# Kernel tuning notes

Hardware: AMD Instinct MI355X
Metric: run time of the kernel (lower is better)

## Reference

```python
import jax, jax.numpy as jnp
import numpy as np

NEG_INF = -1e9
B, D, T_MEL, T_TEXT = 16, 192, 2048, 512


def setup_inputs() -> dict:
    key = jax.random.key(0)
    k1, k2, k3, k4, k5 = jax.random.split(key, 5)
    z_p = jax.random.normal(k1, (B, D, T_MEL), dtype=jnp.float32)
    m_p = jax.random.normal(k2, (B, D, T_TEXT), dtype=jnp.float32)
    logs_p = 0.1 * jax.random.normal(k3, (B, D, T_TEXT), dtype=jnp.float32)
    phoneme_lengths = jax.random.randint(k4, (B,), T_TEXT // 2, T_TEXT + 1, dtype=jnp.int32)
    mel_lengths = jax.random.randint(k5, (B,), T_MEL // 2, T_MEL + 1, dtype=jnp.int32)
    return {"z_p": z_p, "m_p": m_p, "logs_p": logs_p,
            "phoneme_lengths": phoneme_lengths, "mel_lengths": mel_lengths}


def neg_cent_matrix(z_p, m_p, logs_p):
    # z_p: [B,D,Ty] (mel frames), m_p/logs_p: [B,D,Tx] (phonemes)
    s = jnp.exp(-2.0 * logs_p)                                             # 1/sigma^2, [B,D,Tx]
    nc1 = jnp.sum(-0.5 * jnp.log(2.0 * jnp.pi) - logs_p, axis=1, keepdims=True)  # [B,1,Tx]
    nc2 = jnp.einsum('bdy,bdx->byx', -0.5 * z_p * z_p, s)                  # [B,Ty,Tx]
    nc3 = jnp.einsum('bdy,bdx->byx', z_p, m_p * s)                         # [B,Ty,Tx]
    nc4 = jnp.sum(-0.5 * m_p * m_p * s, axis=1, keepdims=True)             # [B,1,Tx]
    return nc1 + nc2 + nc3 + nc4                                           # [B,Ty,Tx]


def maximum_path(neg_cent, t_xs, t_ys):
    """Monotonic alignment search (VITS maximum_path), vmapped over batch.

    neg_cent: [B, T_y, T_x] log-likelihood scores; t_xs/t_ys: valid lengths.
    Returns hard alignment path [B, T_y, T_x] in {0,1}.
    """
    _, T_y, T_x = neg_cent.shape
    x_idx = jnp.arange(T_x)

    def single(value, t_x, t_y):
        # forward DP: cum[y,x] = value[y,x] + max(cum[y-1,x], cum[y-1,x-1])
        init = jnp.where(x_idx == 0, value[0], NEG_INF)

        def fwd_step(prev, v_row):
            shifted = jnp.concatenate([jnp.full((1,), NEG_INF, prev.dtype), prev[:-1]])
            cur = v_row + jnp.maximum(prev, shifted)
            return cur, cur

        _, rest = jax.lax.scan(fwd_step, init, value[1:])
        cum = jnp.concatenate([init[None, :], rest], axis=0)               # [T_y,T_x]

        # backtrack from (t_y-1, t_x-1); rows with y >= t_y are inactive (zeros)
        def bwd_step(index, y):
            active = y < t_y
            row = ((x_idx == index) & active).astype(value.dtype)
            prev_row = cum[jnp.maximum(y - 1, 0)]
            move = (index == y) | (prev_row[index] < prev_row[jnp.maximum(index - 1, 0)])
            move = move & (index > 0) & active & (y > 0)
            nxt = jnp.where(active, index - move.astype(index.dtype), index)
            return nxt, row

        _, rows = jax.lax.scan(bwd_step, t_x - 1, jnp.arange(T_y)[::-1])
        return rows[::-1]

    return jax.vmap(single)(neg_cent, t_xs, t_ys)


def reference(z_p, m_p, logs_p, phoneme_lengths, mel_lengths):
    neg_cent = neg_cent_matrix(z_p, m_p, logs_p)                           # [B,Ty,Tx]
    attn = maximum_path(neg_cent, phoneme_lengths, mel_lengths)            # [B,Ty,Tx]
    T_x = m_p.shape[-1]
    ph_mask = (jnp.arange(T_x)[None, :] < phoneme_lengths[:, None]).astype(z_p.dtype)[:, None, :]  # [B,1,Tx]
    w = jnp.sum(attn, axis=1)[:, None, :]                                  # durations, [B,1,Tx]
    logw_ = jnp.log(w + 1e-6) * ph_mask                                    # [B,1,Tx]
    return neg_cent, attn, logw_
```

## Files before the change

kernel.cpp:

```cpp
#include <hip/hip_runtime.h>
#include <cstdint>
#include <cstddef>

#define B_   16
#define D_   192
#define TY   2048
#define TX   512
#define NEG_INF_F (-1e9f)

#define CHUNK 16
#define RING  4
#define WAVES 8

#define WAITVM(N)  __builtin_amdgcn_s_waitcnt(((N) & 15) | (7 << 4) | (15 << 8) | (((N) >> 4) << 14))
#define WAITLGKM0  __builtin_amdgcn_s_waitcnt(15 | (7 << 4) | (0 << 8) | (3 << 14))

__device__ __forceinline__ void gload_lds16(const float* g, float* l) {
    __builtin_amdgcn_global_load_lds(
        (const __attribute__((address_space(1))) void*)g,
        (__attribute__((address_space(3))) void*)l, 16, 0, 0);
}

__device__ __forceinline__ float dpp_shr1_neginf(float x) {
    int xi  = __builtin_bit_cast(int, x);
    int old = __builtin_bit_cast(int, NEG_INF_F);
    int r = __builtin_amdgcn_update_dpp(old, xi, 0x138, 0xF, 0xF, false);
    return __builtin_bit_cast(float, r);
}

__global__ __launch_bounds__(256)
void nc14_kernel(const float* __restrict__ m_p,
                 const float* __restrict__ logs_p,
                 float* __restrict__ nc14) {
    int gid = blockIdx.x * 256 + threadIdx.x;
    int b = gid >> 9;
    int x = gid & 511;
    const float c = -0.9189385332046727f;
    const float* lp = logs_p + (size_t)b * D_ * TX + x;
    const float* mp = m_p    + (size_t)b * D_ * TX + x;
    float acc1 = 0.f, acc2 = 0.f;
    for (int d = 0; d < D_; ++d) {
        float l = lp[(size_t)d * TX];
        float m = mp[(size_t)d * TX];
        float s = __expf(-2.f * l);
        acc1 += c - l;
        acc2 += m * m * s;
    }
    nc14[gid] = acc1 - 0.5f * acc2;
}

#define BM 128
#define BN 128
#define BK 16

__global__ __launch_bounds__(512)
void gemm_kernel(const float* __restrict__ z_p,
                 const float* __restrict__ m_p,
                 const float* __restrict__ logs_p,
                 const float* __restrict__ nc14,
                 float* __restrict__ out) {
    __shared__ float a_z [BK][BM];
    __shared__ float a_z2[BK][BM];
    __shared__ float sb_s [BK][BN];
    __shared__ float sb_ms[BK][BN];

    const int b  = blockIdx.z;
    const int m0 = blockIdx.y * BM;
    const int n0 = blockIdx.x * BN;
    const int tid = threadIdx.x;
    const int tx = tid & 31;
    const int ty = tid >> 5;

    const int skk = tid >> 5;
    const int sy  = (tid & 31) * 4;

    const float* zb = z_p    + (size_t)b * D_ * TY;
    const float* mb = m_p    + (size_t)b * D_ * TX;
    const float* lb = logs_p + (size_t)b * D_ * TX;

    float acc[8][4];
    #pragma unroll
    for (int i = 0; i < 8; ++i)
        #pragma unroll
        for (int j = 0; j < 4; ++j) acc[i][j] = 0.f;

    float4 va, vlg, vmm;
    auto ld = [&](int k0) {
        va  = *(const float4*)(zb + (size_t)(k0 + skk) * TY + m0 + sy);
        vlg = *(const float4*)(lb + (size_t)(k0 + skk) * TX + n0 + sy);
        vmm = *(const float4*)(mb + (size_t)(k0 + skk) * TX + n0 + sy);
    };
    auto st = [&]() {
        *(float4*)&a_z[skk][sy] = va;
        float4 w;
        w.x = -0.5f * va.x * va.x; w.y = -0.5f * va.y * va.y;
        w.z = -0.5f * va.z * va.z; w.w = -0.5f * va.w * va.w;
        *(float4*)&a_z2[skk][sy] = w;
        float4 s;
        s.x = __expf(-2.f * vlg.x); s.y = __expf(-2.f * vlg.y);
        s.z = __expf(-2.f * vlg.z); s.w = __expf(-2.f * vlg.w);
        *(float4*)&sb_s[skk][sy] = s;
        float4 ms;
        ms.x = vmm.x * s.x; ms.y = vmm.y * s.y;
        ms.z = vmm.z * s.z; ms.w = vmm.w * s.w;
        *(float4*)&sb_ms[skk][sy] = ms;
    };

    ld(0);
    for (int k0 = 0; k0 < D_; k0 += BK) {
        st();
        __syncthreads();
        if (k0 + BK < D_) ld(k0 + BK);
        #pragma unroll
        for (int kk = 0; kk < BK; ++kk) {
            float az[8], a2[8], bs[4], bm[4];
            *(float4*)&az[0] = *(const float4*)&a_z [kk][ty * 8];
            *(float4*)&az[4] = *(const float4*)&a_z [kk][ty * 8 + 4];
            *(float4*)&a2[0] = *(const float4*)&a_z2[kk][ty * 8];
            *(float4*)&a2[4] = *(const float4*)&a_z2[kk][ty * 8 + 4];
            *(float4*)&bs[0] = *(const float4*)&sb_s [kk][tx * 4];
            *(float4*)&bm[0] = *(const float4*)&sb_ms[kk][tx * 4];
            #pragma unroll
            for (int i = 0; i < 8; ++i)
                #pragma unroll
                for (int j = 0; j < 4; ++j)
                    acc[i][j] += a2[i] * bs[j] + az[i] * bm[j];
        }
        __syncthreads();
    }
    const float4 c4 = *(const float4*)(nc14 + b * TX + n0 + tx * 4);
    float* ob = out + (size_t)b * TY * TX + (size_t)m0 * TX + n0 + tx * 4;
    #pragma unroll
    for (int i = 0; i < 8; ++i) {
        float4 r;
        r.x = acc[i][0] + c4.x; r.y = acc[i][1] + c4.y;
        r.z = acc[i][2] + c4.z; r.w = acc[i][3] + c4.w;
        *(float4*)(ob + (size_t)(ty * 8 + i) * TX) = r;
    }
}

__global__ __launch_bounds__(512, 1)
void dp_kernel(float* __restrict__ out,
               const int* __restrict__ t_xs,
               const int* __restrict__ t_ys,
               int* __restrict__ cumE) {
    const size_t PLANE = (size_t)TY * TX;
    const size_t OFF1  = (size_t)B_ * PLANE;
    const size_t OFF2  = 2 * OFF1;

    __shared__ float rows_lds[WAVES][RING][CHUNK * 64];
    __shared__ float bnd[RING][WAVES + 1][CHUNK];
    __shared__ int   w_lds[TX];

    const int b    = blockIdx.x;
    const int tid  = threadIdx.x;
    const int w    = tid >> 6;
    const int lane = tid & 63;
    const int t_x  = t_xs[b];
    const int t_y  = t_ys[b];
    const int tym1 = t_y - 1;
    const int NC   = (t_y + CHUNK - 1) / CHUNK;

    const float* nc   = out + (size_t)b * PLANE;
    float*       attn = out + OFF1 + (size_t)b * PLANE;
    float*       logw = out + OFF2 + (size_t)b * TX;
    unsigned char* bitsb = (unsigned char*)attn;

    w_lds[tid] = 0;
    {
        float* bf = &bnd[0][0][0];
        if (tid < 512) bf[tid] = NEG_INF_F;
        if (tid < 64)  bf[512 + tid] = NEG_INF_F;
    }

    auto issue_chunk = [&](int c) {
        const int slot = c % RING;
        #pragma unroll
        for (int k = 0; k < CHUNK / 4; ++k) {
            int y = c * CHUNK + 4 * k + (lane >> 4);
            if (y > tym1) y = tym1;
            const float* gp = nc + (size_t)y * TX + 64 * w + 4 * (lane & 15);
            gload_lds16(gp, &rows_lds[w][slot][k * 256]);
        }
    };

    float cl = NEG_INF_F;
    const bool lane0  = (lane == 0);
    const bool lane63 = (lane == 63);

    issue_chunk(0);
    issue_chunk(1);
    issue_chunk(2);

    const int ITERS = NC + WAVES - 1;
    for (int i = 0; i < ITERS; ++i) {
        WAITLGKM0;
        __asm__ volatile("" ::: "memory");
        __builtin_amdgcn_s_barrier();
        __asm__ volatile("" ::: "memory");
        const int c = i - w;
        if (c < 0 || c >= NC) continue;
        const bool full = (c + 3 < NC);
        if (full) issue_chunk(c + 3);

        const int pc = c % RING;
        float4 bq0 = *(const float4*)&bnd[pc][w][0];
        float4 bq1 = *(const float4*)&bnd[pc][w][4];
        float4 bq2 = *(const float4*)&bnd[pc][w][8];
        float4 bq3 = *(const float4*)&bnd[pc][w][12];
        float carry = bnd[(c + RING - 1) % RING][w][CHUNK - 1];
        float bv[CHUNK] = {carry,
                           bq0.x, bq0.y, bq0.z, bq0.w,
                           bq1.x, bq1.y, bq1.z, bq1.w,
                           bq2.x, bq2.y, bq2.z, bq2.w,
                           bq3.x, bq3.y, bq3.z};

        if (c >= 3) {
            if (full)               { WAITVM(15); }
            else if (c + 3 == NC)   { WAITVM(11); }
            else if (c + 2 == NC)   { WAITVM(7);  }
            else                    { WAITVM(3);  }
        } else {
            if (c == 0)             { WAITVM(12); }
            else if (c == 1)        { WAITVM(13); }
            else                    { WAITVM(14); }
        }
        __asm__ volatile("" ::: "memory");

        #pragma unroll
        for (int r = 0; r < CHUNK; ++r) __asm__ volatile("" : "+v"(bv[r]));

        const float* vrow = &rows_lds[w][pc][0];
        float vv[CHUNK];
        #pragma unroll
        for (int r = 0; r < CHUNK; ++r) vv[r] = vrow[r * 64 + lane];
        #pragma unroll
        for (int r = 0; r < CHUNK; ++r) __asm__ volatile("" : "+v"(vv[r]));

        const int ybase = c * CHUNK;
        float pub[CHUNK];
        unsigned mlo = 0, mhi = 0;
        #pragma unroll
        for (int r = 0; r < CHUNK; ++r) {
            float sh = dpp_shr1_neginf(cl);
            sh = lane0 ? bv[r] : sh;
            unsigned long long mk = __ballot(cl < sh);
            float cn = vv[r] + fmaxf(cl, sh);
            if (r == 0) {
                float iv = (w == 0 && lane0) ? vv[0] : NEG_INF_F;
                cn = (ybase == 0) ? iv : cn;
            }
            cl = cn;
            pub[r] = cl;
            unsigned lo32 = (unsigned)mk;
            unsigned hi32 = (unsigned)(mk >> 32);
            bool sel = (lane == r);
            mlo = sel ? lo32 : mlo;
            mhi = sel ? hi32 : mhi;
        }
        if (lane63) {
            *(float4*)&bnd[pc][w + 1][0]  = make_float4(pub[0],  pub[1],  pub[2],  pub[3]);
            *(float4*)&bnd[pc][w + 1][4]  = make_float4(pub[4],  pub[5],  pub[6],  pub[7]);
            *(float4*)&bnd[pc][w + 1][8]  = make_float4(pub[8],  pub[9],  pub[10], pub[11]);
            *(float4*)&bnd[pc][w + 1][12] = make_float4(pub[12], pub[13], pub[14], pub[15]);
        }
        {
            const int ys = ybase + lane;
            if (lane < CHUNK && ys < t_y)
                *(uint2*)(bitsb + (size_t)ys * 64 + 8 * w) = make_uint2(mlo, mhi);
        }
    }

    __builtin_amdgcn_s_waitcnt(0);
    __asm__ volatile("" ::: "memory");
    __builtin_amdgcn_s_barrier();
    __asm__ volatile("" ::: "memory");
    if (w != 0) return;

    int idx  = t_x - 1;
    int yhi  = tym1;
    int ytop = tym1;
    int wh   = idx >> 5;

    unsigned vlo = 0, vhi = 0;
    {
        int cnt0 = (ytop >= 31) ? 32 : (ytop + 1);
        int wlo = (wh > 0) ? wh - 1 : 0;
        if (lane < cnt0) {
            const unsigned* rp = (const unsigned*)(bitsb + (size_t)(ytop - lane) * 64);
            vlo = rp[wlo];
            vhi = rp[wh];
        }
    }
    while (ytop >= 0) {
        const int cnt = (ytop >= 31) ? 32 : (ytop + 1);
        unsigned p0 = 0, p1 = 0, p2 = 0;
        const int ynext = ytop - cnt;
        if (ynext >= 0 && lane < 32) {
            int rr = ynext - lane; if (rr < 0) rr = 0;
            const unsigned* rp = (const unsigned*)(bitsb + (size_t)rr * 64);
            const int w2i = wh;
            const int w1i = (wh > 0) ? wh - 1 : 0;
            const int w0i = (wh > 1) ? wh - 2 : 0;
            p0 = rp[w0i]; p1 = rp[w1i]; p2 = rp[w2i];
        }
        const int base  = ((wh > 0) ? wh - 1 : 0) * 32;
        const int idx0  = idx;
        const int yhi0  = yhi;
        unsigned  mask  = 0;
        auto step = [&](int i2) {
            int yy = ytop - i2;
            unsigned lo = (unsigned)__builtin_amdgcn_readlane((int)vlo, i2);
            unsigned hi = (unsigned)__builtin_amdgcn_readlane((int)vhi, i2);
            unsigned long long V = ((unsigned long long)hi << 32) | lo;
            int pos   = idx - base;
            int bit   = (int)((V >> pos) & 1ull);
            int force = (idx == yy) ? 1 : 0;
            int move  = (force | bit) & ((idx > 0) ? 1 : 0) & ((yy > 0) ? 1 : 0);
            mask |= ((unsigned)move) << i2;
            yhi  = move ? (yy - 1) : yhi;
            idx -= move;
        };
        if (cnt == 32) {
            #pragma unroll
            for (int i2 = 0; i2 < 32; ++i2) step(i2);
        } else {
            for (int i2 = 0; i2 < cnt; ++i2) step(i2);
        }
        {
            const int k = lane;
            if (k < 32 && ((mask >> k) & 1u)) {
                unsigned pri = mask & ((1u << k) - 1u);
                int m  = __popc(pri);
                int ph = idx0 - m;
                int dur;
                if (pri) { int kp = 31 - __builtin_clz(pri); dur = k - kp; }
                else     { dur = yhi0 - ytop + k + 1; }
                w_lds[ph] = dur;
            }
        }
        ytop -= cnt;
        if (ytop >= 0) {
            const int whn = idx >> 5;
            vlo = (whn == wh) ? p1 : p0;
            vhi = (whn == wh) ? p2 : p1;
            wh = whn;
        }
    }
    if (lane0) w_lds[idx] = yhi + 1;

    __asm__ volatile("" ::: "memory");
    int v2[8];
    int run = 0;
    #pragma unroll
    for (int j = 0; j < 8; ++j) {
        int wv = w_lds[lane * 8 + j];
        run += wv;
        v2[j] = run;
    }
    int off = run;
    #pragma unroll
    for (int d = 1; d < 64; d <<= 1) {
        int t = __shfl_up(off, d, 64);
        if (lane >= d) off += t;
    }
    int excl = off - run;
    #pragma unroll
    for (int j = 0; j < 8; ++j) {
        int x = lane * 8 + j;
        cumE[b * TX + x] = v2[j] + excl;
        int wv = w_lds[x];
        logw[x] = (x < t_x) ? logf((float)wv + 1e-6f) : 0.f;
    }
}

__global__ __launch_bounds__(256)
void attn_fill_kernel(const int* __restrict__ cumE,
                      float* __restrict__ out) {
    const size_t PLANE = (size_t)TY * TX;
    const size_t OFF1  = (size_t)B_ * PLANE;
    __shared__ int cs[TX + 1];
    const int b  = blockIdx.y;
    const int y0 = blockIdx.x * 4;
    const int t  = threadIdx.x;
    if (t == 0) cs[0] = 0;
    cs[1 + t]       = cumE[b * TX + t];
    cs[1 + 256 + t] = cumE[b * TX + 256 + t];
    __syncthreads();
    const int y  = y0 + (t >> 6);
    const int x0 = (t & 63) * 8;
    float r[8];
    #pragma unroll
    for (int j = 0; j < 8; ++j)
        r[j] = (cs[x0 + j] <= y && y < cs[x0 + j + 1]) ? 1.f : 0.f;
    float* p = out + OFF1 + (size_t)b * PLANE + (size_t)y * TX + x0;
    *(float4*)p       = *(float4*)&r[0];
    *(float4*)(p + 4) = *(float4*)&r[4];
}

extern "C" void kernel_launch(void* const* d_in, const int* in_sizes, int n_in,
                              void* d_out, int out_size, void* d_ws, size_t ws_size,
                              hipStream_t stream) {
    const float* z_p    = (const float*)d_in[0];
    const float* m_p    = (const float*)d_in[1];
    const float* logs_p = (const float*)d_in[2];
    const int* ph_len   = (const int*)d_in[3];
    const int* mel_len  = (const int*)d_in[4];
    float* out  = (float*)d_out;
    float* nc14 = (float*)d_ws;
    int*   cumE = (int*)d_ws;

    nc14_kernel<<<(B_ * TX) / 256, 256, 0, stream>>>(m_p, logs_p, nc14);
    gemm_kernel<<<dim3(TX / BN, TY / BM, B_), 512, 0, stream>>>(z_p, m_p, logs_p, nc14, out);
    dp_kernel<<<B_, WAVES * 64, 0, stream>>>(out, ph_len, mel_len, cumE);
    attn_fill_kernel<<<dim3(TY / 4, B_), 256, 0, stream>>>(cumE, out);
}
```

Baseline: 701.8 us.

## Prefetch next chunk's LDS rows and carry into registers during current DP step

The forward DP loop now double-buffers the per-chunk value rows and the carry value in two register arrays. After computing the current chunk, each wave waits for the next chunk's global-to-LDS load and reads it into the alternate register set, so LDS read latency is moved off the critical path at the start of the next iteration. The loop is unrolled by two with swapped buffers, and the vmcnt wait thresholds are retuned to match the new issue order. This costs extra VGPRs and adds risk in the correctness of the wait counts and of reading the carry before the barrier.

```diff
diff --git a/kernel.cpp b/kernel.cpp
--- a/kernel.cpp
+++ b/kernel.cpp
@@ -192,82 +192,108 @@
     issue_chunk(1);
     issue_chunk(2);
 
+    float vvA[CHUNK], vvB[CHUNK];
+    float carryA = NEG_INF_F, carryB = NEG_INF_F;
+    #pragma unroll
+    for (int r = 0; r < CHUNK; ++r) { vvA[r] = 0.f; vvB[r] = 0.f; }
+
+    if (w == 0) {
+        WAITVM(8);
+        __asm__ volatile("" ::: "memory");
+        const float* vn = &rows_lds[0][0][0];
+        #pragma unroll
+        for (int r = 0; r < CHUNK; ++r) vvA[r] = vn[r * 64 + lane];
+        #pragma unroll
+        for (int r = 0; r < CHUNK; ++r) __asm__ volatile("" : "+v"(vvA[r]));
+    }
+
     const int ITERS = NC + WAVES - 1;
-    for (int i = 0; i < ITERS; ++i) {
+
+    auto body = [&](float (&vvc)[CHUNK], float& carryc,
+                    float (&vvn)[CHUNK], float& carryn, int i) {
         WAITLGKM0;
         __asm__ volatile("" ::: "memory");
         __builtin_amdgcn_s_barrier();
         __asm__ volatile("" ::: "memory");
         const int c = i - w;
-        if (c < 0 || c >= NC) continue;
-        const bool full = (c + 3 < NC);
-        if (full) issue_chunk(c + 3);
-
-        const int pc = c % RING;
-        float4 bq0 = *(const float4*)&bnd[pc][w][0];
-        float4 bq1 = *(const float4*)&bnd[pc][w][4];
-        float4 bq2 = *(const float4*)&bnd[pc][w][8];
-        float4 bq3 = *(const float4*)&bnd[pc][w][12];
-        float carry = bnd[(c + RING - 1) % RING][w][CHUNK - 1];
-        float bv[CHUNK] = {carry,
-                           bq0.x, bq0.y, bq0.z, bq0.w,
-                           bq1.x, bq1.y, bq1.z, bq1.w,
-                           bq2.x, bq2.y, bq2.z, bq2.w,
-                           bq3.x, bq3.y, bq3.z};
-
-        if (c >= 3) {
-            if (full)               { WAITVM(15); }
-            else if (c + 3 == NC)   { WAITVM(11); }
-            else if (c + 2 == NC)   { WAITVM(7);  }
+        if (c >= 0 && c < NC) {
+            if (c + 3 < NC) issue_chunk(c + 3);
+            const int pc = c % RING;
+            float4 bq0 = *(const float4*)&bnd[pc][w][0];
+            float4 bq1 = *(const float4*)&bnd[pc][w][4];
+            float4 bq2 = *(const float4*)&bnd[pc][w][8];
+            float4 bq3 = *(const float4*)&bnd[pc][w][12];
+
+            const int ybase = c * CHUNK;
+            float pub[CHUNK];
+            unsigned mlo = 0, mhi = 0;
+            {
+                float sh = dpp_shr1_neginf(cl);
+                sh = lane0 ? carryc : sh;
+                unsigned long long mk = __ballot(cl < sh);
+                float cn = vvc[0] + fmaxf(cl, sh);
+                if (ybase == 0)
+                    cn = (w == 0 && lane0) ? vvc[0] : NEG_INF_F;
+                cl = cn;
+                pub[0] = cl;
+                bool sel = (lane == 0);
+                mlo = sel ? (unsigned)mk : mlo;
+                mhi = sel ? (unsigned)(mk >> 32) : mhi;
+            }
+            float bv1[CHUNK - 1] = {bq0.x, bq0.y, bq0.z, bq0.w,
+                                    bq1.x, bq1.y, bq1.z, bq1.w,
+                                    bq2.x, bq2.y, bq2.z, bq2.w,
+                                    bq3.x, bq3.y, bq3.z};
+            #pragma unroll
+            for (int r = 1; r < CHUNK; ++r) {
+                float sh = dpp_shr1_neginf(cl);
+                sh = lane0 ? bv1[r - 1] : sh;
+                unsigned long long mk = __ballot(cl < sh);
+                float cn = vvc[r] + fmaxf(cl, sh);
+                cl = cn;
+                pub[r] = cl;
+                bool sel = (lane == r);
+                mlo = sel ? (unsigned)mk : mlo;
+                mhi = sel ? (unsigned)(mk >> 32) : mhi;
+            }
+            if (lane63) {
+                *(float4*)&bnd[pc][w + 1][0]  = make_float4(pub[0],  pub[1],  pub[2],  pub[3]);
+                *(float4*)&bnd[pc][w + 1][4]  = make_float4(pub[4],  pub[5],  pub[6],  pub[7]);
+                *(float4*)&bnd[pc][w + 1][8]  = make_float4(pub[8],  pub[9],  pub[10], pub[11]);
+                *(float4*)&bnd[pc][w + 1][12] = make_float4(pub[12], pub[13], pub[14], pub[15]);
+            }
+            {
+                const int ys = ybase + lane;
+                if (lane < CHUNK && ys < t_y)
+                    *(uint2*)(bitsb + (size_t)ys * 64 + 8 * w) = make_uint2(mlo, mhi);
+            }
+        }
+        const int cp = (i - w) + 1;
+        if (cp >= 0 && cp < NC) {
+            const int cc = cp - 1;
+            if (cp == 0)            { WAITVM(8);  }
+            else if (cp == 1)       { WAITVM(9);  }
+            else if (cp == 2)       { WAITVM(10); }
+            else if (cc + 4 <= NC)  { WAITVM(11); }
+            else if (cc + 3 == NC)  { WAITVM(7);  }
             else                    { WAITVM(3);  }
-        } else {
-            if (c == 0)             { WAITVM(12); }
-            else if (c == 1)        { WAITVM(13); }
-            else                    { WAITVM(14); }
-        }
-        __asm__ volatile("" ::: "memory");
-
-        #pragma unroll
-        for (int r = 0; r < CHUNK; ++r) __asm__ volatile("" : "+v"(bv[r]));
-
-        const float* vrow = &rows_lds[w][pc][0];
-        float vv[CHUNK];
-        #pragma unroll
-        for (int r = 0; r < CHUNK; ++r) vv[r] = vrow[r * 64 + lane];
-        #pragma unroll
-        for (int r = 0; r < CHUNK; ++r) __asm__ volatile("" : "+v"(vv[r]));
-
-        const int ybase = c * CHUNK;
-        float pub[CHUNK];
-        unsigned mlo = 0, mhi = 0;
-        #pragma unroll
-        for (int r = 0; r < CHUNK; ++r) {
-            float sh = dpp_shr1_neginf(cl);
-            sh = lane0 ? bv[r] : sh;
-            unsigned long long mk = __ballot(cl < sh);
-            float cn = vv[r] + fmaxf(cl, sh);
-            if (r == 0) {
-                float iv = (w == 0 && lane0) ? vv[0] : NEG_INF_F;
-                cn = (ybase == 0) ? iv : cn;
-            }
-            cl = cn;
-            pub[r] = cl;
-            unsigned lo32 = (unsigned)mk;
-            unsigned hi32 = (unsigned)(mk >> 32);
-            bool sel = (lane == r);
-            mlo = sel ? lo32 : mlo;
-            mhi = sel ? hi32 : mhi;
-        }
-        if (lane63) {
-            *(float4*)&bnd[pc][w + 1][0]  = make_float4(pub[0],  pub[1],  pub[2],  pub[3]);
-            *(float4*)&bnd[pc][w + 1][4]  = make_float4(pub[4],  pub[5],  pub[6],  pub[7]);
-            *(float4*)&bnd[pc][w + 1][8]  = make_float4(pub[8],  pub[9],  pub[10], pub[11]);
-            *(float4*)&bnd[pc][w + 1][12] = make_float4(pub[12], pub[13], pub[14], pub[15]);
-        }
-        {
-            const int ys = ybase + lane;
-            if (lane < CHUNK && ys < t_y)
-                *(uint2*)(bitsb + (size_t)ys * 64 + 8 * w) = make_uint2(mlo, mhi);
+            __asm__ volatile("" ::: "memory");
+            const float* vn = &rows_lds[w][cp % RING][0];
+            #pragma unroll
+            for (int r = 0; r < CHUNK; ++r) vvn[r] = vn[r * 64 + lane];
+            carryn = bnd[(cp + RING - 1) % RING][w][CHUNK - 1];
+            #pragma unroll
+            for (int r = 0; r < CHUNK; ++r) __asm__ volatile("" : "+v"(vvn[r]));
+            __asm__ volatile("" : "+v"(carryn));
+        }
+    };
+
+    {
+        int i = 0;
+        while (i < ITERS) {
+            body(vvA, carryA, vvB, carryB, i); ++i;
+            if (i >= ITERS) break;
+            body(vvB, carryB, vvA, carryA, i); ++i;
         }
     }
 
```

Measured after the change: 678.3 us. -3.3%, faster.
